# Optimization experiments

Hardware: AMD Instinct MI355X
Metric: run time of the kernel (lower is better)

Reference implementation:

```python
import jax, jax.numpy as jnp
import numpy as np

MASK_W = 1.0
KPT_W = 0.5

SOBEL_X = jnp.array([[-1.0, 0.0, 1.0], [-2.0, 0.0, 2.0], [-1.0, 0.0, 1.0]], jnp.float32).reshape(1, 1, 3, 3)
SOBEL_Y = jnp.array([[-1.0, -2.0, -1.0], [0.0, 0.0, 0.0], [1.0, 2.0, 1.0]], jnp.float32).reshape(1, 1, 3, 3)
BOX = jnp.ones((1, 1, 3, 3), jnp.float32)


def conv3x3(x, k):
    # x: [N,1,H,W]; torch F.conv2d is cross-correlation, same as lax conv
    return jax.lax.conv_general_dilated(
        x, k, window_strides=(1, 1), padding=[(1, 1), (1, 1)],
        dimension_numbers=('NCHW', 'OIHW', 'NCHW'))


def sobel_edge(mask):
    ex = conv3x3(mask, SOBEL_X)
    ey = conv3x3(mask, SOBEL_Y)
    return jnp.sqrt(ex * ex + ey * ey)


def grid_sample_bilinear_zeros(img, grid):
    # img: [H,W]; grid: [K,2] in [-1,1], (x,y) order; align_corners=False, zero padding
    H, W = img.shape
    x = (grid[:, 0] + 1.0) * (W * 0.5) - 0.5
    y = (grid[:, 1] + 1.0) * (H * 0.5) - 0.5
    x0 = jnp.floor(x).astype(jnp.int32)
    y0 = jnp.floor(y).astype(jnp.int32)
    x1 = x0 + 1
    y1 = y0 + 1
    wx1 = x - x0.astype(x.dtype)
    wx0 = 1.0 - wx1
    wy1 = y - y0.astype(y.dtype)
    wy0 = 1.0 - wy1

    def gather(ix, iy):
        valid = (ix >= 0) & (ix < W) & (iy >= 0) & (iy < H)
        v = img[jnp.clip(iy, 0, H - 1), jnp.clip(ix, 0, W - 1)]
        return jnp.where(valid, v, 0.0)

    return (wx0 * wy0 * gather(x0, y0) + wx1 * wy0 * gather(x1, y0)
            + wx0 * wy1 * gather(x0, y1) + wx1 * wy1 * gather(x1, y1))


def setup_inputs() -> dict:
    key = jax.random.key(0)
    k1, k2, k3, k4 = jax.random.split(key, 4)
    return {
        'pred_keypoints': jax.random.uniform(k1, (1024, 2), jnp.float32),
        'target_keypoints': jax.random.uniform(k2, (1024, 2), jnp.float32),
        'pred_seg': jax.random.uniform(k3, (1, 1, 4096, 4096), jnp.float32),
        'target_seg': jax.random.uniform(k4, (1, 1, 4096, 4096), jnp.float32),
    }


def reference(pred_keypoints, target_keypoints, pred_seg, target_seg):
    target_edge = sobel_edge(target_seg)
    pred_edge = sobel_edge(pred_seg)
    edge_loss = jnp.mean((pred_edge - target_edge) ** 2)
    distance_map = conv3x3(pred_edge, BOX)  # [1,1,H,W]
    kd = grid_sample_bilinear_zeros(distance_map[0, 0], pred_keypoints)  # [K]
    constraint_loss = jnp.mean(kd)
    return MASK_W * edge_loss + KPT_W * constraint_loss
```

## Files before the change

### kernel.cpp

```cpp
#include <hip/hip_runtime.h>

#define H 4096
#define W 4096
#define TH 4
#define NR (TH + 2)
#define BX 256
#define GX 4
#define GY (H / TH)
#define NEDGE (GX * GY)
#define NKPB 16

#define MASK_W 1.0f
#define KPT_W 0.5f

struct Prep { float dx0, dx1, dx2, dx3, s0, s1, s2, s3; };

__device__ __forceinline__ float fast_sqrt(float x) {
    return __builtin_amdgcn_sqrtf(x);
}

__device__ __forceinline__ Prep fin(float4 v, float h, bool isL, bool isR) {
    float lf = __shfl_up(v.w, 1);
    float rf = __shfl_down(v.x, 1);
    lf = isL ? h : lf;
    rf = isR ? h : rf;
    Prep o;
    o.dx0 = v.y - lf;
    o.dx1 = v.z - v.x;
    o.dx2 = v.w - v.y;
    o.dx3 = rf  - v.z;
    o.s0 = __fmaf_rn(2.f, v.x, lf  + v.y);
    o.s1 = __fmaf_rn(2.f, v.y, v.x + v.z);
    o.s2 = __fmaf_rn(2.f, v.z, v.y + v.w);
    o.s3 = __fmaf_rn(2.f, v.w, v.z + rf);
    return o;
}

__device__ __forceinline__ float edge1(float dxA, float dxB, float dxC, float sA, float sC) {
    float ex = dxA + __fmaf_rn(2.f, dxB, dxC);
    float ey = sC - sA;
    return fast_sqrt(__fmaf_rn(ex, ex, ey * ey));
}

__global__ __launch_bounds__(BX) void fused_kernel(const float* __restrict__ pred,
                                                   const float* __restrict__ targ,
                                                   const float* __restrict__ kp,
                                                   float* __restrict__ ws) {
    int bid = blockIdx.x;

    if (bid < NEDGE) {
        int gx = bid & (GX - 1);
        int gy = bid >> 2;
        int c  = gx * (BX * 4) + threadIdx.x * 4;
        int r0 = gy * TH;
        int lane = threadIdx.x & 63;
        bool isL = (lane == 0), isR = (lane == 63);
        bool haloCol = (isL & (c > 0)) | (isR & (c + 4 < W));

        const float* bp = pred + (size_t)r0 * W + c;
        const float* bt = targ + (size_t)r0 * W + c;

        float4 pv[NR], tv[NR];
        float  hp[NR], ht[NR];
        #pragma unroll
        for (int r = 0; r < NR; ++r) {
            int row = r0 - 1 + r;
            bool valid = (unsigned)row < (unsigned)H;
            const float* pp = bp + (ptrdiff_t)(r - 1) * W;
            const float* tt = bt + (ptrdiff_t)(r - 1) * W;
            pv[r] = valid ? *(const float4*)pp : make_float4(0.f, 0.f, 0.f, 0.f);
            tv[r] = valid ? *(const float4*)tt : make_float4(0.f, 0.f, 0.f, 0.f);
            float h1 = 0.f, h2 = 0.f;
            if (valid & haloCol) {
                const float* q1 = isL ? pp - 1 : pp + 4;
                const float* q2 = isL ? tt - 1 : tt + 4;
                h1 = *q1; h2 = *q2;
            }
            hp[r] = h1; ht[r] = h2;
        }

        Prep pA = fin(pv[0], hp[0], isL, isR);
        Prep tA = fin(tv[0], ht[0], isL, isR);
        Prep pB = fin(pv[1], hp[1], isL, isR);
        Prep tB = fin(tv[1], ht[1], isL, isR);

        float acc = 0.f;
        #pragma unroll
        for (int i = 0; i < TH; ++i) {
            Prep pC = fin(pv[i + 2], hp[i + 2], isL, isR);
            Prep tC = fin(tv[i + 2], ht[i + 2], isL, isR);

            float pe, te, d;
            pe = edge1(pA.dx0, pB.dx0, pC.dx0, pA.s0, pC.s0);
            te = edge1(tA.dx0, tB.dx0, tC.dx0, tA.s0, tC.s0);
            d = pe - te; acc = __fmaf_rn(d, d, acc);
            pe = edge1(pA.dx1, pB.dx1, pC.dx1, pA.s1, pC.s1);
            te = edge1(tA.dx1, tB.dx1, tC.dx1, tA.s1, tC.s1);
            d = pe - te; acc = __fmaf_rn(d, d, acc);
            pe = edge1(pA.dx2, pB.dx2, pC.dx2, pA.s2, pC.s2);
            te = edge1(tA.dx2, tB.dx2, tC.dx2, tA.s2, tC.s2);
            d = pe - te; acc = __fmaf_rn(d, d, acc);
            pe = edge1(pA.dx3, pB.dx3, pC.dx3, pA.s3, pC.s3);
            te = edge1(tA.dx3, tB.dx3, tC.dx3, tA.s3, tC.s3);
            d = pe - te; acc = __fmaf_rn(d, d, acc);

            pA = pB; pB = pC;
            tA = tB; tB = tC;
        }

        #pragma unroll
        for (int m = 32; m; m >>= 1) acc += __shfl_xor(acc, m);

        __shared__ float wsum[BX / 64];
        if ((threadIdx.x & 63) == 0) wsum[threadIdx.x >> 6] = acc;
        __syncthreads();
        if (threadIdx.x == 0) {
            float s = 0.f;
            #pragma unroll
            for (int i = 0; i < BX / 64; ++i) s += wsum[i];
            ws[bid] = s;
        }
    } else {
        int t = threadIdx.x;
        if (t >= 64) return;
        int k = (bid - NEDGE) * 64 + t;

        float gx = kp[2 * k];
        float gy = kp[2 * k + 1];
        float x = (gx + 1.f) * (W * 0.5f) - 0.5f;
        float y = (gy + 1.f) * (H * 0.5f) - 0.5f;
        float fx0 = floorf(x), fy0 = floorf(y);
        int x0 = (int)fx0, y0 = (int)fy0;
        int x1 = x0 + 1, y1 = y0 + 1;
        float wx1 = x - fx0, wx0 = 1.f - wx1;
        float wy1 = y - fy0, wy0 = 1.f - wy1;

        float sg[6][6];
        #pragma unroll
        for (int i = 0; i < 6; ++i) {
            int rr = y0 - 2 + i;
            #pragma unroll
            for (int j = 0; j < 6; ++j) {
                int cc = x0 - 2 + j;
                bool ok = (rr >= 0) & (rr < H) & (cc >= 0) & (cc < W);
                sg[i][j] = ok ? pred[(size_t)rr * W + cc] : 0.f;
            }
        }

        float e[4][4];
        #pragma unroll
        for (int i = 0; i < 4; ++i) {
            int rr = y0 - 1 + i;
            #pragma unroll
            for (int j = 0; j < 4; ++j) {
                int cc = x0 - 1 + j;
                if (rr < 0 || rr >= H || cc < 0 || cc >= W) { e[i][j] = 0.f; continue; }
                float ex = (sg[i][j + 2] - sg[i][j])
                         + 2.f * (sg[i + 1][j + 2] - sg[i + 1][j])
                         + (sg[i + 2][j + 2] - sg[i + 2][j]);
                float ey = (sg[i + 2][j] + 2.f * sg[i + 2][j + 1] + sg[i + 2][j + 2])
                         - (sg[i][j] + 2.f * sg[i][j + 1] + sg[i][j + 2]);
                e[i][j] = fast_sqrt(__fmaf_rn(ex, ex, ey * ey));
            }
        }

        float dmap[2][2];
        #pragma unroll
        for (int a = 0; a < 2; ++a) {
            #pragma unroll
            for (int b = 0; b < 2; ++b) {
                float s = 0.f;
                #pragma unroll
                for (int i = 0; i < 3; ++i)
                    #pragma unroll
                    for (int j = 0; j < 3; ++j) s += e[a + i][b + j];
                dmap[a][b] = s;
            }
        }

        bool vx0 = (x0 >= 0) & (x0 < W), vx1 = (x1 >= 0) & (x1 < W);
        bool vy0 = (y0 >= 0) & (y0 < H), vy1 = (y1 >= 0) & (y1 < H);
        float v00 = (vx0 & vy0) ? dmap[0][0] : 0.f;
        float v01 = (vx1 & vy0) ? dmap[0][1] : 0.f;
        float v10 = (vx0 & vy1) ? dmap[1][0] : 0.f;
        float v11 = (vx1 & vy1) ? dmap[1][1] : 0.f;
        float kd = wx0 * wy0 * v00 + wx1 * wy0 * v01
                 + wx0 * wy1 * v10 + wx1 * wy1 * v11;

        #pragma unroll
        for (int m = 32; m; m >>= 1) kd += __shfl_xor(kd, m);
        if (t == 0) ws[NEDGE + (bid - NEDGE)] = kd;
    }
}

__global__ __launch_bounds__(256) void final_kernel(const float* __restrict__ ws,
                                                    float* __restrict__ out) {
    int t = threadIdx.x;
    float es = 0.f;
    #pragma unroll
    for (int i = 0; i < NEDGE / 256; ++i) es += ws[t + i * 256];
    float ks = (t < NKPB) ? ws[NEDGE + t] : 0.f;

    #pragma unroll
    for (int m = 32; m; m >>= 1) {
        es += __shfl_xor(es, m);
        ks += __shfl_xor(ks, m);
    }
    __shared__ float res[4], rks[4];
    int wid = t >> 6;
    if ((t & 63) == 0) { res[wid] = es; rks[wid] = ks; }
    __syncthreads();
    if (t == 0) {
        float e2 = res[0] + res[1] + res[2] + res[3];
        float k2 = rks[0] + rks[1] + rks[2] + rks[3];
        float edge_loss = e2 * (1.f / ((float)H * (float)W));
        float constraint_loss = k2 * (1.f / 1024.f);
        out[0] = MASK_W * edge_loss + KPT_W * constraint_loss;
    }
}

extern "C" void kernel_launch(void* const* d_in, const int* in_sizes, int n_in,
                              void* d_out, int out_size, void* d_ws, size_t ws_size,
                              hipStream_t stream) {
    const float* kp   = (const float*)d_in[0];
    const float* pred = (const float*)d_in[2];
    const float* targ = (const float*)d_in[3];
    float* out = (float*)d_out;
    float* ws  = (float*)d_ws;

    fused_kernel<<<NEDGE + NKPB, BX, 0, stream>>>(pred, targ, kp, ws);
    final_kernel<<<1, 256, 0, stream>>>(ws, out);
}
```

Baseline: 154.6 us.

## Process four row tiles per block with double-buffered register prefetch

```diff
diff --git a/kernel.cpp b/kernel.cpp
--- a/kernel.cpp
+++ b/kernel.cpp
@@ -7,16 +7,41 @@
 #define BX 256
 #define GX 4
 #define GY (H / TH)
-#define NEDGE (GX * GY)
+#define NTILE (GX * GY)
+#define TPB 4
+#define NEDGE (NTILE / TPB)
 #define NKPB 16
 
 #define MASK_W 1.0f
 #define KPT_W 0.5f
 
 struct Prep { float dx0, dx1, dx2, dx3, s0, s1, s2, s3; };
+struct TileBuf { float4 pv[NR], tv[NR]; float hp[NR], ht[NR]; };
 
 __device__ __forceinline__ float fast_sqrt(float x) {
     return __builtin_amdgcn_sqrtf(x);
+}
+
+__device__ __forceinline__ void load_tile(TileBuf& b,
+                                          const float* __restrict__ bp,
+                                          const float* __restrict__ bt,
+                                          int r0, bool haloCol, bool isL) {
+    #pragma unroll
+    for (int r = 0; r < NR; ++r) {
+        int row = r0 - 1 + r;
+        bool valid = (unsigned)row < (unsigned)H;
+        const float* pp = bp + (ptrdiff_t)row * W;
+        const float* tt = bt + (ptrdiff_t)row * W;
+        b.pv[r] = valid ? *(const float4*)pp : make_float4(0.f, 0.f, 0.f, 0.f);
+        b.tv[r] = valid ? *(const float4*)tt : make_float4(0.f, 0.f, 0.f, 0.f);
+        float h1 = 0.f, h2 = 0.f;
+        if (valid & haloCol) {
+            const float* q1 = isL ? pp - 1 : pp + 4;
+            const float* q2 = isL ? tt - 1 : tt + 4;
+            h1 = *q1; h2 = *q2;
+        }
+        b.hp[r] = h1; b.ht[r] = h2;
+    }
 }
 
 __device__ __forceinline__ Prep fin(float4 v, float h, bool isL, bool isR) {
@@ -42,6 +67,34 @@
     return fast_sqrt(__fmaf_rn(ex, ex, ey * ey));
 }
 
+__device__ __forceinline__ float compute_tile(const TileBuf& b, bool isL, bool isR, float acc) {
+    Prep pA = fin(b.pv[0], b.hp[0], isL, isR);
+    Prep tA = fin(b.tv[0], b.ht[0], isL, isR);
+    Prep pB = fin(b.pv[1], b.hp[1], isL, isR);
+    Prep tB = fin(b.tv[1], b.ht[1], isL, isR);
+    #pragma unroll
+    for (int i = 0; i < TH; ++i) {
+        Prep pC = fin(b.pv[i + 2], b.hp[i + 2], isL, isR);
+        Prep tC = fin(b.tv[i + 2], b.ht[i + 2], isL, isR);
+        float pe, te, d;
+        pe = edge1(pA.dx0, pB.dx0, pC.dx0, pA.s0, pC.s0);
+        te = edge1(tA.dx0, tB.dx0, tC.dx0, tA.s0, tC.s0);
+        d = pe - te; acc = __fmaf_rn(d, d, acc);
+        pe = edge1(pA.dx1, pB.dx1, pC.dx1, pA.s1, pC.s1);
+        te = edge1(tA.dx1, tB.dx1, tC.dx1, tA.s1, tC.s1);
+        d = pe - te; acc = __fmaf_rn(d, d, acc);
+        pe = edge1(pA.dx2, pB.dx2, pC.dx2, pA.s2, pC.s2);
+        te = edge1(tA.dx2, tB.dx2, tC.dx2, tA.s2, tC.s2);
+        d = pe - te; acc = __fmaf_rn(d, d, acc);
+        pe = edge1(pA.dx3, pB.dx3, pC.dx3, pA.s3, pC.s3);
+        te = edge1(tA.dx3, tB.dx3, tC.dx3, tA.s3, tC.s3);
+        d = pe - te; acc = __fmaf_rn(d, d, acc);
+        pA = pB; pB = pC;
+        tA = tB; tB = tC;
+    }
+    return acc;
+}
+
 __global__ __launch_bounds__(BX) void fused_kernel(const float* __restrict__ pred,
                                                    const float* __restrict__ targ,
                                                    const float* __restrict__ kp,
@@ -50,63 +103,26 @@
 
     if (bid < NEDGE) {
         int gx = bid & (GX - 1);
-        int gy = bid >> 2;
+        int gyb = (bid >> 2) * TPB;
         int c  = gx * (BX * 4) + threadIdx.x * 4;
-        int r0 = gy * TH;
         int lane = threadIdx.x & 63;
         bool isL = (lane == 0), isR = (lane == 63);
         bool haloCol = (isL & (c > 0)) | (isR & (c + 4 < W));
 
-        const float* bp = pred + (size_t)r0 * W + c;
-        const float* bt = targ + (size_t)r0 * W + c;
-
-        float4 pv[NR], tv[NR];
-        float  hp[NR], ht[NR];
-        #pragma unroll
-        for (int r = 0; r < NR; ++r) {
-            int row = r0 - 1 + r;
-            bool valid = (unsigned)row < (unsigned)H;
-            const float* pp = bp + (ptrdiff_t)(r - 1) * W;
-            const float* tt = bt + (ptrdiff_t)(r - 1) * W;
-            pv[r] = valid ? *(const float4*)pp : make_float4(0.f, 0.f, 0.f, 0.f);
-            tv[r] = valid ? *(const float4*)tt : make_float4(0.f, 0.f, 0.f, 0.f);
-            float h1 = 0.f, h2 = 0.f;
-            if (valid & haloCol) {
-                const float* q1 = isL ? pp - 1 : pp + 4;
-                const float* q2 = isL ? tt - 1 : tt + 4;
-                h1 = *q1; h2 = *q2;
-            }
-            hp[r] = h1; ht[r] = h2;
-        }
-
-        Prep pA = fin(pv[0], hp[0], isL, isR);
-        Prep tA = fin(tv[0], ht[0], isL, isR);
-        Prep pB = fin(pv[1], hp[1], isL, isR);
-        Prep tB = fin(tv[1], ht[1], isL, isR);
-
+        const float* bp = pred + c;
+        const float* bt = targ + c;
+
+        TileBuf A, B;
         float acc = 0.f;
-        #pragma unroll
-        for (int i = 0; i < TH; ++i) {
-            Prep pC = fin(pv[i + 2], hp[i + 2], isL, isR);
-            Prep tC = fin(tv[i + 2], ht[i + 2], isL, isR);
-
-            float pe, te, d;
-            pe = edge1(pA.dx0, pB.dx0, pC.dx0, pA.s0, pC.s0);
-            te = edge1(tA.dx0, tB.dx0, tC.dx0, tA.s0, tC.s0);
-            d = pe - te; acc = __fmaf_rn(d, d, acc);
-            pe = edge1(pA.dx1, pB.dx1, pC.dx1, pA.s1, pC.s1);
-            te = edge1(tA.dx1, tB.dx1, tC.dx1, tA.s1, tC.s1);
-            d = pe - te; acc = __fmaf_rn(d, d, acc);
-            pe = edge1(pA.dx2, pB.dx2, pC.dx2, pA.s2, pC.s2);
-            te = edge1(tA.dx2, tB.dx2, tC.dx2, tA.s2, tC.s2);
-            d = pe - te; acc = __fmaf_rn(d, d, acc);
-            pe = edge1(pA.dx3, pB.dx3, pC.dx3, pA.s3, pC.s3);
-            te = edge1(tA.dx3, tB.dx3, tC.dx3, tA.s3, tC.s3);
-            d = pe - te; acc = __fmaf_rn(d, d, acc);
-
-            pA = pB; pB = pC;
-            tA = tB; tB = tC;
-        }
+
+        load_tile(A, bp, bt, (gyb + 0) * TH, haloCol, isL);
+        load_tile(B, bp, bt, (gyb + 1) * TH, haloCol, isL);
+        acc = compute_tile(A, isL, isR, acc);
+        load_tile(A, bp, bt, (gyb + 2) * TH, haloCol, isL);
+        acc = compute_tile(B, isL, isR, acc);
+        load_tile(B, bp, bt, (gyb + 3) * TH, haloCol, isL);
+        acc = compute_tile(A, isL, isR, acc);
+        acc = compute_tile(B, isL, isR, acc);
 
         #pragma unroll
         for (int m = 32; m; m >>= 1) acc += __shfl_xor(acc, m);
```

Result: slower. 168.2 us (+8.8%).

## Stage edge tiles into LDS via async global_load_lds and schedule keypoint blocks first

Applied to the files above, without the earlier changes.

```diff
diff --git a/kernel.cpp b/kernel.cpp
--- a/kernel.cpp
+++ b/kernel.cpp
@@ -5,10 +5,11 @@
 #define TH 4
 #define NR (TH + 2)
 #define BX 256
-#define GX 4
+#define STRIPS 4
 #define GY (H / TH)
-#define NEDGE (GX * GY)
+#define NEDGE (STRIPS * GY)
 #define NKPB 16
+#define SIDEOFF (2 * NR * 1024)
 
 #define MASK_W 1.0f
 #define KPT_W 0.5f
@@ -19,11 +20,19 @@
     return __builtin_amdgcn_sqrtf(x);
 }
 
-__device__ __forceinline__ Prep fin(float4 v, float h, bool isL, bool isR) {
-    float lf = __shfl_up(v.w, 1);
-    float rf = __shfl_down(v.x, 1);
-    lf = isL ? h : lf;
-    rf = isR ? h : rf;
+__device__ __forceinline__ void async_cp16(const float* g, float* l) {
+    __builtin_amdgcn_global_load_lds(
+        (const __attribute__((address_space(1))) void*)g,
+        (__attribute__((address_space(3))) void*)l,
+        16, 0, 0);
+}
+
+__device__ __forceinline__ Prep mkprep(const float* smem, int m, int sr, int t, bool rowok) {
+    if (!rowok) { Prep z = {0.f,0.f,0.f,0.f,0.f,0.f,0.f,0.f}; return z; }
+    int base = ((m * NR + sr) << 10);
+    float4 v = *(const float4*)&smem[base + (t << 2)];
+    float lf = (t == 0)      ? smem[SIDEOFF + (m*NR+sr)*2 + 0] : smem[base + (t << 2) - 1];
+    float rf = (t == BX - 1) ? smem[SIDEOFF + (m*NR+sr)*2 + 1] : smem[base + (t << 2) + 4];
     Prep o;
     o.dx0 = v.y - lf;
     o.dx1 = v.z - v.x;
@@ -46,49 +55,63 @@
                                                    const float* __restrict__ targ,
                                                    const float* __restrict__ kp,
                                                    float* __restrict__ ws) {
+    __shared__ float smem[SIDEOFF + 2 * NR * 2];
     int bid = blockIdx.x;
 
-    if (bid < NEDGE) {
-        int gx = bid & (GX - 1);
-        int gy = bid >> 2;
-        int c  = gx * (BX * 4) + threadIdx.x * 4;
+    if (bid >= NKPB) {
+        int ebid = bid - NKPB;
+        int gx = ebid & (STRIPS - 1);
+        int gy = ebid >> 2;
+        int c0 = gx << 10;
         int r0 = gy * TH;
-        int lane = threadIdx.x & 63;
-        bool isL = (lane == 0), isR = (lane == 63);
-        bool haloCol = (isL & (c > 0)) | (isR & (c + 4 < W));
-
-        const float* bp = pred + (size_t)r0 * W + c;
-        const float* bt = targ + (size_t)r0 * W + c;
-
-        float4 pv[NR], tv[NR];
-        float  hp[NR], ht[NR];
-        #pragma unroll
-        for (int r = 0; r < NR; ++r) {
-            int row = r0 - 1 + r;
-            bool valid = (unsigned)row < (unsigned)H;
-            const float* pp = bp + (ptrdiff_t)(r - 1) * W;
-            const float* tt = bt + (ptrdiff_t)(r - 1) * W;
-            pv[r] = valid ? *(const float4*)pp : make_float4(0.f, 0.f, 0.f, 0.f);
-            tv[r] = valid ? *(const float4*)tt : make_float4(0.f, 0.f, 0.f, 0.f);
-            float h1 = 0.f, h2 = 0.f;
-            if (valid & haloCol) {
-                const float* q1 = isL ? pp - 1 : pp + 4;
-                const float* q2 = isL ? tt - 1 : tt + 4;
-                h1 = *q1; h2 = *q2;
-            }
-            hp[r] = h1; ht[r] = h2;
-        }
-
-        Prep pA = fin(pv[0], hp[0], isL, isR);
-        Prep tA = fin(tv[0], ht[0], isL, isR);
-        Prep pB = fin(pv[1], hp[1], isL, isR);
-        Prep tB = fin(tv[1], ht[1], isL, isR);
+        int t  = threadIdx.x;
+        int w  = t >> 6, lane = t & 63;
+
+        #pragma unroll
+        for (int jj = 0; jj < 12; ++jj) {
+            int j  = w * 12 + jj;
+            int m  = j / 24;
+            int rr = (j % 24) >> 2;
+            int q  = j & 3;
+            int rg = r0 - 1 + rr;
+            rg = rg < 0 ? 0 : (rg > H - 1 ? H - 1 : rg);
+            const float* g = (m ? targ : pred) + (size_t)rg * W + c0 + (q << 8) + (lane << 2);
+            float* l = &smem[((m * NR + rr) << 10) + (q << 8)];
+            async_cp16(g, l);
+        }
+
+        if (t == 0 || t == BX - 1) {
+            bool right = (t == BX - 1);
+            int col = right ? c0 + 1024 : c0 - 1;
+            bool cok = (unsigned)col < (unsigned)W;
+            #pragma unroll
+            for (int m = 0; m < 2; ++m) {
+                #pragma unroll
+                for (int rr = 0; rr < NR; ++rr) {
+                    int rg = r0 - 1 + rr;
+                    bool ok = cok & ((unsigned)rg < (unsigned)H);
+                    int rgc = rg < 0 ? 0 : (rg > H - 1 ? H - 1 : rg);
+                    float v = ok ? (m ? targ : pred)[(size_t)rgc * W + col] : 0.f;
+                    smem[SIDEOFF + (m * NR + rr) * 2 + (right ? 1 : 0)] = v;
+                }
+            }
+        }
+        __syncthreads();
+
+        bool ok0 = (r0 > 0);
+        bool ok5 = (r0 + TH < H);
+
+        Prep pA = mkprep(smem, 0, 0, t, ok0);
+        Prep tA = mkprep(smem, 1, 0, t, ok0);
+        Prep pB = mkprep(smem, 0, 1, t, true);
+        Prep tB = mkprep(smem, 1, 1, t, true);
 
         float acc = 0.f;
         #pragma unroll
         for (int i = 0; i < TH; ++i) {
-            Prep pC = fin(pv[i + 2], hp[i + 2], isL, isR);
-            Prep tC = fin(tv[i + 2], ht[i + 2], isL, isR);
+            bool rok = (i + 2 < NR - 1) ? true : ok5;
+            Prep pC = mkprep(smem, 0, i + 2, t, rok);
+            Prep tC = mkprep(smem, 1, i + 2, t, rok);
 
             float pe, te, d;
             pe = edge1(pA.dx0, pB.dx0, pC.dx0, pA.s0, pC.s0);
@@ -112,18 +135,18 @@
         for (int m = 32; m; m >>= 1) acc += __shfl_xor(acc, m);
 
         __shared__ float wsum[BX / 64];
-        if ((threadIdx.x & 63) == 0) wsum[threadIdx.x >> 6] = acc;
+        if ((t & 63) == 0) wsum[t >> 6] = acc;
         __syncthreads();
-        if (threadIdx.x == 0) {
+        if (t == 0) {
             float s = 0.f;
             #pragma unroll
             for (int i = 0; i < BX / 64; ++i) s += wsum[i];
-            ws[bid] = s;
+            ws[ebid] = s;
         }
     } else {
         int t = threadIdx.x;
         if (t >= 64) return;
-        int k = (bid - NEDGE) * 64 + t;
+        int k = bid * 64 + t;
 
         float gx = kp[2 * k];
         float gy = kp[2 * k + 1];
@@ -189,7 +212,7 @@
 
         #pragma unroll
         for (int m = 32; m; m >>= 1) kd += __shfl_xor(kd, m);
-        if (t == 0) ws[NEDGE + (bid - NEDGE)] = kd;
+        if (t == 0) ws[NEDGE + bid] = kd;
     }
 }
 
```

Result: slower. 175.8 us (+13.7%).

## Stream taller row strips with float2 columns and fold keypoint work into edge blocks

Applied to the files above, without the earlier changes.

```diff
diff --git a/kernel.cpp b/kernel.cpp
--- a/kernel.cpp
+++ b/kernel.cpp
@@ -2,37 +2,45 @@
 
 #define H 4096
 #define W 4096
-#define TH 4
-#define NR (TH + 2)
+#define TR 16
 #define BX 256
-#define GX 4
-#define GY (H / TH)
-#define NEDGE (GX * GY)
+#define SW 512
+#define NSTRIP (W / SW)
+#define GY (H / TR)
+#define NB (NSTRIP * GY)
 #define NKPB 16
+#define KPOFF NB
 
 #define MASK_W 1.0f
 #define KPT_W 0.5f
 
-struct Prep { float dx0, dx1, dx2, dx3, s0, s1, s2, s3; };
-
-__device__ __forceinline__ float fast_sqrt(float x) {
-    return __builtin_amdgcn_sqrtf(x);
-}
-
-__device__ __forceinline__ Prep fin(float4 v, float h, bool isL, bool isR) {
-    float lf = __shfl_up(v.w, 1);
-    float rf = __shfl_down(v.x, 1);
-    lf = isL ? h : lf;
-    rf = isR ? h : rf;
-    Prep o;
-    o.dx0 = v.y - lf;
-    o.dx1 = v.z - v.x;
-    o.dx2 = v.w - v.y;
-    o.dx3 = rf  - v.z;
-    o.s0 = __fmaf_rn(2.f, v.x, lf  + v.y);
-    o.s1 = __fmaf_rn(2.f, v.y, v.x + v.z);
-    o.s2 = __fmaf_rn(2.f, v.z, v.y + v.w);
-    o.s3 = __fmaf_rn(2.f, v.w, v.z + rf);
+struct Raw2 { float x, y, h; };
+struct Prep2 { float dx0, dx1, s0, s1; };
+
+__device__ __forceinline__ float fast_sqrt(float v) {
+    return __builtin_amdgcn_sqrtf(v);
+}
+
+__device__ __forceinline__ Raw2 load2(const float* __restrict__ p, bool rvalid,
+                                      bool hval, bool isL) {
+    Raw2 r;
+    if (rvalid) { float2 v = *(const float2*)p; r.x = v.x; r.y = v.y; }
+    else        { r.x = 0.f; r.y = 0.f; }
+    r.h = 0.f;
+    if (rvalid & hval) r.h = isL ? p[-1] : p[2];
+    return r;
+}
+
+__device__ __forceinline__ Prep2 fin2(const Raw2& r, bool isL, bool isR) {
+    float lf = __shfl_up(r.y, 1);
+    float rf = __shfl_down(r.x, 1);
+    lf = isL ? r.h : lf;
+    rf = isR ? r.h : rf;
+    Prep2 o;
+    o.dx0 = r.y - lf;
+    o.dx1 = rf  - r.x;
+    o.s0 = __fmaf_rn(2.f, r.x, lf  + r.y);
+    o.s1 = __fmaf_rn(2.f, r.y, r.x + rf);
     return o;
 }
 
@@ -42,154 +50,140 @@
     return fast_sqrt(__fmaf_rn(ex, ex, ey * ey));
 }
 
-__global__ __launch_bounds__(BX) void fused_kernel(const float* __restrict__ pred,
-                                                   const float* __restrict__ targ,
-                                                   const float* __restrict__ kp,
-                                                   float* __restrict__ ws) {
+__global__ __launch_bounds__(BX, 8) void fused_kernel(const float* __restrict__ pred,
+                                                      const float* __restrict__ targ,
+                                                      const float* __restrict__ kp,
+                                                      float* __restrict__ ws) {
     int bid = blockIdx.x;
-
-    if (bid < NEDGE) {
-        int gx = bid & (GX - 1);
-        int gy = bid >> 2;
-        int c  = gx * (BX * 4) + threadIdx.x * 4;
-        int r0 = gy * TH;
-        int lane = threadIdx.x & 63;
-        bool isL = (lane == 0), isR = (lane == 63);
-        bool haloCol = (isL & (c > 0)) | (isR & (c + 4 < W));
-
-        const float* bp = pred + (size_t)r0 * W + c;
-        const float* bt = targ + (size_t)r0 * W + c;
-
-        float4 pv[NR], tv[NR];
-        float  hp[NR], ht[NR];
-        #pragma unroll
-        for (int r = 0; r < NR; ++r) {
-            int row = r0 - 1 + r;
-            bool valid = (unsigned)row < (unsigned)H;
-            const float* pp = bp + (ptrdiff_t)(r - 1) * W;
-            const float* tt = bt + (ptrdiff_t)(r - 1) * W;
-            pv[r] = valid ? *(const float4*)pp : make_float4(0.f, 0.f, 0.f, 0.f);
-            tv[r] = valid ? *(const float4*)tt : make_float4(0.f, 0.f, 0.f, 0.f);
-            float h1 = 0.f, h2 = 0.f;
-            if (valid & haloCol) {
-                const float* q1 = isL ? pp - 1 : pp + 4;
-                const float* q2 = isL ? tt - 1 : tt + 4;
-                h1 = *q1; h2 = *q2;
-            }
-            hp[r] = h1; ht[r] = h2;
-        }
-
-        Prep pA = fin(pv[0], hp[0], isL, isR);
-        Prep tA = fin(tv[0], ht[0], isL, isR);
-        Prep pB = fin(pv[1], hp[1], isL, isR);
-        Prep tB = fin(tv[1], ht[1], isL, isR);
-
-        float acc = 0.f;
-        #pragma unroll
-        for (int i = 0; i < TH; ++i) {
-            Prep pC = fin(pv[i + 2], hp[i + 2], isL, isR);
-            Prep tC = fin(tv[i + 2], ht[i + 2], isL, isR);
-
-            float pe, te, d;
-            pe = edge1(pA.dx0, pB.dx0, pC.dx0, pA.s0, pC.s0);
-            te = edge1(tA.dx0, tB.dx0, tC.dx0, tA.s0, tC.s0);
-            d = pe - te; acc = __fmaf_rn(d, d, acc);
-            pe = edge1(pA.dx1, pB.dx1, pC.dx1, pA.s1, pC.s1);
-            te = edge1(tA.dx1, tB.dx1, tC.dx1, tA.s1, tC.s1);
-            d = pe - te; acc = __fmaf_rn(d, d, acc);
-            pe = edge1(pA.dx2, pB.dx2, pC.dx2, pA.s2, pC.s2);
-            te = edge1(tA.dx2, tB.dx2, tC.dx2, tA.s2, tC.s2);
-            d = pe - te; acc = __fmaf_rn(d, d, acc);
-            pe = edge1(pA.dx3, pB.dx3, pC.dx3, pA.s3, pC.s3);
-            te = edge1(tA.dx3, tB.dx3, tC.dx3, tA.s3, tC.s3);
-            d = pe - te; acc = __fmaf_rn(d, d, acc);
-
-            pA = pB; pB = pC;
-            tA = tB; tB = tC;
-        }
-
-        #pragma unroll
-        for (int m = 32; m; m >>= 1) acc += __shfl_xor(acc, m);
-
-        __shared__ float wsum[BX / 64];
-        if ((threadIdx.x & 63) == 0) wsum[threadIdx.x >> 6] = acc;
-        __syncthreads();
-        if (threadIdx.x == 0) {
-            float s = 0.f;
-            #pragma unroll
-            for (int i = 0; i < BX / 64; ++i) s += wsum[i];
-            ws[bid] = s;
-        }
-    } else {
-        int t = threadIdx.x;
-        if (t >= 64) return;
-        int k = (bid - NEDGE) * 64 + t;
-
-        float gx = kp[2 * k];
-        float gy = kp[2 * k + 1];
-        float x = (gx + 1.f) * (W * 0.5f) - 0.5f;
-        float y = (gy + 1.f) * (H * 0.5f) - 0.5f;
+    int t   = threadIdx.x;
+    int lane = t & 63;
+
+    if (bid < NKPB && t < 64) {
+        int k = bid * 64 + t;
+        float gxx = kp[2 * k];
+        float gyy = kp[2 * k + 1];
+        float x = (gxx + 1.f) * (W * 0.5f) - 0.5f;
+        float y = (gyy + 1.f) * (H * 0.5f) - 0.5f;
         float fx0 = floorf(x), fy0 = floorf(y);
         int x0 = (int)fx0, y0 = (int)fy0;
         int x1 = x0 + 1, y1 = y0 + 1;
         float wx1 = x - fx0, wx0 = 1.f - wx1;
         float wy1 = y - fy0, wy0 = 1.f - wy1;
 
-        float sg[6][6];
-        #pragma unroll
-        for (int i = 0; i < 6; ++i) {
-            int rr = y0 - 2 + i;
+        float s0r[6], s1r[6], s2r[6];
+        #pragma unroll
+        for (int j = 0; j < 6; ++j) {
+            int cc = x0 - 2 + j;
+            bool okc = (cc >= 0) & (cc < W);
+            int r_ = y0 - 2;
+            bool ok0 = okc & (r_ >= 0) & (r_ < H);
+            s0r[j] = ok0 ? pred[(size_t)r_ * W + cc] : 0.f;
+            int r1_ = y0 - 1;
+            bool ok1 = okc & (r1_ >= 0) & (r1_ < H);
+            s1r[j] = ok1 ? pred[(size_t)r1_ * W + cc] : 0.f;
+        }
+        float dm00 = 0.f, dm01 = 0.f, dm10 = 0.f, dm11 = 0.f;
+        #pragma unroll
+        for (int i = 0; i < 4; ++i) {
+            int r2_ = y0 + i;
             #pragma unroll
             for (int j = 0; j < 6; ++j) {
                 int cc = x0 - 2 + j;
-                bool ok = (rr >= 0) & (rr < H) & (cc >= 0) & (cc < W);
-                sg[i][j] = ok ? pred[(size_t)rr * W + cc] : 0.f;
+                bool ok = (cc >= 0) & (cc < W) & (r2_ >= 0) & (r2_ < H);
+                s2r[j] = ok ? pred[(size_t)r2_ * W + cc] : 0.f;
             }
-        }
-
-        float e[4][4];
-        #pragma unroll
-        for (int i = 0; i < 4; ++i) {
             int rr = y0 - 1 + i;
+            bool rok = (rr >= 0) & (rr < H);
+            float e[4];
             #pragma unroll
             for (int j = 0; j < 4; ++j) {
                 int cc = x0 - 1 + j;
-                if (rr < 0 || rr >= H || cc < 0 || cc >= W) { e[i][j] = 0.f; continue; }
-                float ex = (sg[i][j + 2] - sg[i][j])
-                         + 2.f * (sg[i + 1][j + 2] - sg[i + 1][j])
-                         + (sg[i + 2][j + 2] - sg[i + 2][j]);
-                float ey = (sg[i + 2][j] + 2.f * sg[i + 2][j + 1] + sg[i + 2][j + 2])
-                         - (sg[i][j] + 2.f * sg[i][j + 1] + sg[i][j + 2]);
-                e[i][j] = fast_sqrt(__fmaf_rn(ex, ex, ey * ey));
+                bool ok = rok & (cc >= 0) & (cc < W);
+                float ex = (s0r[j + 2] - s0r[j])
+                         + 2.f * (s1r[j + 2] - s1r[j])
+                         + (s2r[j + 2] - s2r[j]);
+                float ey = (s2r[j] + 2.f * s2r[j + 1] + s2r[j + 2])
+                         - (s0r[j] + 2.f * s0r[j + 1] + s0r[j + 2]);
+                e[j] = ok ? fast_sqrt(__fmaf_rn(ex, ex, ey * ey)) : 0.f;
             }
-        }
-
-        float dmap[2][2];
-        #pragma unroll
-        for (int a = 0; a < 2; ++a) {
+            float c0s = e[0] + e[1] + e[2];
+            float c1s = e[1] + e[2] + e[3];
+            if (i <= 2) { dm00 += c0s; dm01 += c1s; }
+            if (i >= 1) { dm10 += c0s; dm11 += c1s; }
             #pragma unroll
-            for (int b = 0; b < 2; ++b) {
-                float s = 0.f;
-                #pragma unroll
-                for (int i = 0; i < 3; ++i)
-                    #pragma unroll
-                    for (int j = 0; j < 3; ++j) s += e[a + i][b + j];
-                dmap[a][b] = s;
-            }
+            for (int j = 0; j < 6; ++j) { s0r[j] = s1r[j]; s1r[j] = s2r[j]; }
         }
 
         bool vx0 = (x0 >= 0) & (x0 < W), vx1 = (x1 >= 0) & (x1 < W);
         bool vy0 = (y0 >= 0) & (y0 < H), vy1 = (y1 >= 0) & (y1 < H);
-        float v00 = (vx0 & vy0) ? dmap[0][0] : 0.f;
-        float v01 = (vx1 & vy0) ? dmap[0][1] : 0.f;
-        float v10 = (vx0 & vy1) ? dmap[1][0] : 0.f;
-        float v11 = (vx1 & vy1) ? dmap[1][1] : 0.f;
+        float v00 = (vx0 & vy0) ? dm00 : 0.f;
+        float v01 = (vx1 & vy0) ? dm01 : 0.f;
+        float v10 = (vx0 & vy1) ? dm10 : 0.f;
+        float v11 = (vx1 & vy1) ? dm11 : 0.f;
         float kd = wx0 * wy0 * v00 + wx1 * wy0 * v01
                  + wx0 * wy1 * v10 + wx1 * wy1 * v11;
-
         #pragma unroll
         for (int m = 32; m; m >>= 1) kd += __shfl_xor(kd, m);
-        if (t == 0) ws[NEDGE + (bid - NEDGE)] = kd;
+        if (t == 0) ws[KPOFF + bid] = kd;
+    }
+
+    int sx = bid & (NSTRIP - 1);
+    int gy = bid >> 3;
+    int c  = (sx << 9) + (t << 1);
+    int r0 = gy * TR;
+    bool isL = (lane == 0), isR = (lane == 63);
+    bool hval = (isL & (c > 0)) | (isR & (c + 2 < W));
+
+    const float* pr = pred + (ptrdiff_t)(r0 - 1) * W + c;
+    const float* tr = targ + (ptrdiff_t)(r0 - 1) * W + c;
+
+    Raw2 rpA = load2(pr, r0 > 0, hval, isL); pr += W;
+    Raw2 rtA = load2(tr, r0 > 0, hval, isL); tr += W;
+    Raw2 rpB = load2(pr, true,   hval, isL); pr += W;
+    Raw2 rtB = load2(tr, true,   hval, isL); tr += W;
+    Raw2 rpn = load2(pr, true,   hval, isL); pr += W;
+    Raw2 rtn = load2(tr, true,   hval, isL); tr += W;
+
+    Prep2 pA = fin2(rpA, isL, isR);
+    Prep2 tA = fin2(rtA, isL, isR);
+    Prep2 pB = fin2(rpB, isL, isR);
+    Prep2 tB = fin2(rtB, isL, isR);
+
+    float acc = 0.f;
+    #pragma unroll
+    for (int i = 0; i < TR; ++i) {
+        Raw2 rpc = rpn, rtc = rtn;
+        if (i < TR - 1) {
+            bool nv = (r0 + i + 2) < H;
+            rpn = load2(pr, nv, hval, isL); pr += W;
+            rtn = load2(tr, nv, hval, isL); tr += W;
+        }
+        Prep2 pC = fin2(rpc, isL, isR);
+        Prep2 tC = fin2(rtc, isL, isR);
+
+        float pe, te, d;
+        pe = edge1(pA.dx0, pB.dx0, pC.dx0, pA.s0, pC.s0);
+        te = edge1(tA.dx0, tB.dx0, tC.dx0, tA.s0, tC.s0);
+        d = pe - te; acc = __fmaf_rn(d, d, acc);
+        pe = edge1(pA.dx1, pB.dx1, pC.dx1, pA.s1, pC.s1);
+        te = edge1(tA.dx1, tB.dx1, tC.dx1, tA.s1, tC.s1);
+        d = pe - te; acc = __fmaf_rn(d, d, acc);
+
+        pA = pB; pB = pC;
+        tA = tB; tB = tC;
+    }
+
+    #pragma unroll
+    for (int m = 32; m; m >>= 1) acc += __shfl_xor(acc, m);
+
+    __shared__ float wsum[BX / 64];
+    if ((t & 63) == 0) wsum[t >> 6] = acc;
+    __syncthreads();
+    if (t == 0) {
+        float s = 0.f;
+        #pragma unroll
+        for (int i = 0; i < BX / 64; ++i) s += wsum[i];
+        ws[bid] = s;
     }
 }
 
@@ -198,8 +192,8 @@
     int t = threadIdx.x;
     float es = 0.f;
     #pragma unroll
-    for (int i = 0; i < NEDGE / 256; ++i) es += ws[t + i * 256];
-    float ks = (t < NKPB) ? ws[NEDGE + t] : 0.f;
+    for (int i = 0; i < NB / 256; ++i) es += ws[t + i * 256];
+    float ks = (t < NKPB) ? ws[KPOFF + t] : 0.f;
 
     #pragma unroll
     for (int m = 32; m; m >>= 1) {
@@ -228,6 +222,6 @@
     float* out = (float*)d_out;
     float* ws  = (float*)d_ws;
 
-    fused_kernel<<<NEDGE + NKPB, BX, 0, stream>>>(pred, targ, kp, ws);
+    fused_kernel<<<NB, BX, 0, stream>>>(pred, targ, kp, ws);
     final_kernel<<<1, 256, 0, stream>>>(ws, out);
 }
```

Measured after the change: 309.4 us. 2x slower.
